# Performance work log

Hardware: AMD Instinct MI355X
Metric: run time of the kernel (lower is better)

## Reference

```python
import jax, jax.numpy as jnp
import numpy as np

B, T, DIM = 512, 243, 512
C = DIM // 2      # 256 channels per branch
CH = C // 2       # 128 hidden channels in ECL (cdiv=2)


def layer_norm(x, g, b, eps=1e-5):
    m = jnp.mean(x, axis=-1, keepdims=True)
    v = jnp.var(x, axis=-1, keepdims=True)
    return (x - m) * jax.lax.rsqrt(v + eps) * g + b


def gconv(x_btc, w):
    # grouped conv1d (groups=2), kernel 3, pad 1, no bias; x: [B,T,Cin], w: [Cout, Cin//2, 3]
    x = jnp.transpose(x_btc, (0, 2, 1))  # NCH
    y = jax.lax.conv_general_dilated(
        x, w, window_strides=(1,), padding=[(1, 1)],
        dimension_numbers=('NCH', 'OIH', 'NCH'), feature_group_count=2)
    return jnp.transpose(y, (0, 2, 1))


def setup_inputs() -> dict:
    key = jax.random.key(0)
    ks = jax.random.split(key, 4)
    F = (T + 1) // 2  # 122 == T//2+1 for odd T
    return {
        'x': jax.random.normal(ks[0], (B, T, DIM), dtype=jnp.float32),
        'lfilter': jax.random.normal(ks[1], (F, T // 2 + 1, 2), dtype=jnp.float32) * 0.02,
        'w1': jax.random.normal(ks[2], (CH, C // 2, 3), dtype=jnp.float32) * 0.05,
        'w2': jax.random.normal(ks[3], (C, CH // 2, 3), dtype=jnp.float32) * 0.05,
        'g1': jnp.ones((CH,), jnp.float32),
        'b1': jnp.zeros((CH,), jnp.float32),
        'g2': jnp.ones((C,), jnp.float32),
        'b2': jnp.zeros((C,), jnp.float32),
    }


def reference(x, lfilter, w1, w2, g1, b1, g2, b2):
    res, gate = jnp.split(x, 2, axis=-1)  # each [B, T, C]
    # GlobalFilter: rfft -> learned complex matmul over frequency axis -> irfft
    X = jnp.fft.rfft(res.astype(jnp.float32), n=T, axis=1, norm='ortho')  # [B, T//2+1, C] complex
    lf = lfilter[..., 0] + 1j * lfilter[..., 1]  # [(T+1)//2, T//2+1]
    X = jnp.einsum('fk,bkc->bfc', lf, X)
    res = jnp.fft.irfft(X, n=T, axis=1, norm='ortho')  # [B, T, C]
    # ECL gating branch
    h = gconv(gate, w1)                                  # [B, T, CH]
    h = jax.nn.gelu(layer_norm(h, g1, b1), approximate=False)
    h = gconv(h, w2)                                     # [B, T, C]
    h = jax.nn.sigmoid(layer_norm(h, g2, b2))
    gate = gate * h
    return jnp.concatenate([res, gate], axis=-1)
```

## Files before the change

### kernel.cpp

```cpp
#include <hip/hip_runtime.h>
#include <math.h>

typedef unsigned short ushort_t;
typedef unsigned int uint_t;
typedef __attribute__((ext_vector_type(8))) short short8v;
typedef __attribute__((ext_vector_type(4))) float f32x4;

#define BB   512
#define TT   243
#define DIMV 512
#define CC   256
#define CHH  128
#define FF   122
#define NKK  122

__device__ __forceinline__ float b2f(ushort_t u) {
  union { uint_t i; float f; } z; z.i = ((uint_t)u) << 16; return z.f;
}
__device__ __forceinline__ ushort_t f2b(float f) {
  union { float f; uint_t i; } z; z.f = f;
  uint_t r = (z.i + 0x7fffu + ((z.i >> 16) & 1u)) >> 16;
  return (ushort_t)r;
}
__device__ __forceinline__ uint_t pack2(float a, float b) {
  uint_t r;
  asm("v_cvt_pk_bf16_f32 %0, %1, %2" : "=v"(r) : "v"(a), "v"(b));
  return r;
}
__device__ __forceinline__ float gelu_f(float x) {
  float z = fabsf(x) * 0.70710678118654752f;
  float t = __builtin_amdgcn_rcpf(fmaf(0.3275911f, z, 1.0f));
  float p = fmaf(1.061405429f, t, -1.453152027f);
  p = fmaf(p, t, 1.421413741f);
  p = fmaf(p, t, -0.284496736f);
  p = fmaf(p, t, 0.254829592f);
  p = p * t;
  float e = __expf(-z * z);
  float erfa = 1.0f - p * e;
  float erfs = copysignf(erfa, x);
  return 0.5f * x * (1.0f + erfs);
}
__device__ __forceinline__ float sigmoid_f(float x) {
  return __builtin_amdgcn_rcpf(1.0f + __expf(-x));
}
union FragU { uint_t u[4]; short8v s; };


__global__ __launch_bounds__(256) void k_prep1(const float* __restrict__ lf, float* __restrict__ A,
    const float* __restrict__ w1, const float* __restrict__ w2,
    ushort_t* __restrict__ w1f, ushort_t* __restrict__ w2f) {
  __shared__ float2 tab[TT];
  int bid = blockIdx.x;
  if (bid < FF) {
    int f = bid;
    int tp = threadIdx.x;
    if (tp < TT) {
      float s, c;
      sincosf(6.28318530717958647692f * (float)tp / (float)TT, &s, &c);
      tab[tp] = make_float2(s, c);
    }
    __syncthreads();
    if (tp >= TT) return;
    float are = 0.f, aim = 0.f;
    int m = 0;
    const float* lrow = lf + (size_t)f * NKK * 2;
    for (int k = 0; k < NKK; ++k) {
      float2 sc = tab[m];
      float lr = lrow[2 * k], li = lrow[2 * k + 1];
      are = fmaf(lr, sc.y, fmaf(li, sc.x, are));
      aim = fmaf(li, sc.y, fmaf(-lr, sc.x, aim));
      m += tp; if (m >= TT) m -= TT;
    }
    A[(f * TT + tp) * 2 + 0] = are;
    A[(f * TT + tp) * 2 + 1] = aim;
  } else {
    int q = (bid - FF) * 256 + threadIdx.x;
    if (q < 49152) {
      int j = q & 7, l = (q >> 3) & 63, ot = (q >> 9) & 3, rest = q >> 11;
      int ks = rest % 12, g = rest / 12;
      int o = ot * 16 + (l & 15);
      int k = ks * 32 + 8 * (l >> 4) + j;
      int dk = k >> 7, i = k & 127;
      w1f[q] = f2b(w1[(g * 64 + o) * 384 + i * 3 + dk]);
    } else if (q < 98304) {
      int q2 = q - 49152;
      int j = q2 & 7, l = (q2 >> 3) & 63, ot = (q2 >> 9) & 7, rest = q2 >> 12;
      int ks = rest % 6, g = rest / 6;
      int o = ot * 16 + (l & 15);
      int k = ks * 32 + 8 * (l >> 4) + j;
      int dk = k >> 6, i = k & 63;
      w2f[q2] = f2b(w2[(g * 128 + o) * 192 + i * 3 + dk]);
    }
  }
}

__global__ void k_compute_M(const float* __restrict__ A, ushort_t* __restrict__ Ffrag) {
  __shared__ float2 tab[TT];
  int t = blockIdx.x;
  int tp = threadIdx.x;
  if (tp < TT) {
    float s, c;
    sincosf(6.28318530717958647692f * (float)tp / (float)TT, &s, &c);
    tab[tp] = make_float2(s, c);
  }
  __syncthreads();
  float val = 0.f;
  if (t < TT && tp < TT) {
    float acc = A[tp * 2 + 0];
    int m = t;
    for (int f = 1; f < FF; ++f) {
      float2 sc = tab[m];
      float ar = A[(f * TT + tp) * 2 + 0];
      float ai = A[(f * TT + tp) * 2 + 1];
      acc = fmaf(2.f * ar, sc.y, fmaf(-2.f * ai, sc.x, acc));
      m += t; if (m >= TT) m -= TT;
    }
    val = acc * (1.0f / (float)TT);
  }
  int kstep = tp >> 5, ko = tp & 31, p = ko >> 3, j = ko & 7;
  int mt = t >> 4, row = t & 15, lane = p * 16 + row;
  Ffrag[(((kstep * 16 + mt) * 64) + lane) * 8 + j] = f2b(val);
}


#define RST   129
#define BT    32
#define NTIL  8
#define XROWS 36
#define XSTD  130
#define HROWS 34
#define HSTD  66
#define GXS_OFF  0
#define GHS_OFF  4680
#define GRED_OFF 6924
#define SMEM_DW  8256

__device__ __forceinline__ void res_path(int rid, uint_t* smem,
    const float* __restrict__ x, const ushort_t* __restrict__ Ffrag, float* __restrict__ out) {
  uint_t* xs = smem;
  int b = rid >> 2, c0 = (rid & 3) * 64;
  int tid = threadIdx.x, l = tid & 63, w = tid >> 6;
  const float* xb = x + (size_t)b * TT * DIMV + c0;
  const short8v* Fp = (const short8v*)Ffrag;

  int cc = tid & 63, kp0 = tid >> 6;
#pragma unroll 8
  for (int it = 0; it < 32; ++it) {
    int kp = kp0 + 4 * it, tp = 2 * kp;
    float v0 = (tp < TT) ? xb[(size_t)tp * DIMV + cc] : 0.f;
    float v1 = (tp + 1 < TT) ? xb[(size_t)(tp + 1) * DIMV + cc] : 0.f;
    xs[cc * RST + kp] = pack2(v0, v1);
  }
  __syncthreads();

  f32x4 acc[4][4];
#pragma unroll
  for (int q = 0; q < 4; ++q)
#pragma unroll
    for (int m = 0; m < 4; ++m) acc[q][m] = (f32x4){0.f, 0.f, 0.f, 0.f};

#pragma unroll 2
  for (int ks = 0; ks < 8; ++ks) {
    FragU bfr[4];
#pragma unroll
    for (int q = 0; q < 4; ++q) bfr[q].s = Fp[(ks * 16 + 4 * w + q) * 64 + l];
#pragma unroll
    for (int m = 0; m < 4; ++m) {
      FragU af;
      const uint_t* pp = &xs[(16 * m + (l & 15)) * RST + ks * 16 + 4 * (l >> 4)];
      af.u[0] = pp[0]; af.u[1] = pp[1]; af.u[2] = pp[2]; af.u[3] = pp[3];
#pragma unroll
      for (int q = 0; q < 4; ++q)
        acc[q][m] = __builtin_amdgcn_mfma_f32_16x16x32_bf16(af.s, bfr[q].s, acc[q][m], 0, 0, 0);
    }
  }

  float* ob = out + (size_t)b * TT * DIMV + c0;
#pragma unroll
  for (int q = 0; q < 4; ++q) {
    int t = (4 * w + q) * 16 + (l & 15);
    if (t < TT) {
#pragma unroll
      for (int m = 0; m < 4; ++m)
        *(f32x4*)&ob[(size_t)t * DIMV + 16 * m + 4 * (l >> 4)] = acc[q][m];
    }
  }
}

__device__ __forceinline__ void gate_path(int gid, uint_t* smem,
    const float* __restrict__ x,
    const ushort_t* __restrict__ w1f, const float* __restrict__ g1, const float* __restrict__ b1,
    const ushort_t* __restrict__ w2f, const float* __restrict__ g2, const float* __restrict__ b2,
    float* __restrict__ out) {
  uint_t* xs = smem + GXS_OFF;
  uint_t* hs = smem + GHS_OFF;
  float* red1s = (float*)(smem + GRED_OFF);
  float* red1q = red1s + 192;
  float* red2s = red1q + 192;
  float* red2q = red2s + 128;
  int b = gid >> 3, t0 = (gid & 7) * BT;
  int tid = threadIdx.x, l = tid & 63, w = tid >> 6;
  int g = w >> 1, half = w & 1;

  const float* xb = x + (size_t)b * TT * DIMV + CC;
#pragma unroll 3
  for (int it = 0; it < 9; ++it) {
    int e = tid + it * 256;
    int r = e >> 6, cq = e & 63;
    int t = t0 - 2 + r;
    float4 v = make_float4(0.f, 0.f, 0.f, 0.f);
    if (t >= 0 && t < TT) v = *(const float4*)&xb[(size_t)t * DIMV + 4 * cq];
    *(uint2*)&xs[r * XSTD + 2 * cq] = make_uint2(pack2(v.x, v.y), pack2(v.z, v.w));
  }
  __syncthreads();

  const short8v* w1p = (const short8v*)w1f;
  int gdw = g * 64;
  f32x4 acc1[2][3];
#pragma unroll
  for (int a = 0; a < 2; ++a)
#pragma unroll
    for (int nt = 0; nt < 3; ++nt) acc1[a][nt] = (f32x4){0.f, 0.f, 0.f, 0.f};

#pragma unroll 2
  for (int ks = 0; ks < 12; ++ks) {
    short8v af[2];
#pragma unroll
    for (int a = 0; a < 2; ++a)
      af[a] = w1p[((g * 12 + ks) * 4 + half * 2 + a) * 64 + l];
    int dk = ks >> 2, i0dw = (ks & 3) * 16;
    FragU bf[3];
#pragma unroll
    for (int nt = 0; nt < 3; ++nt) {
      int row = (l & 15) + 16 * nt + dk;
      if (nt == 2) row = row > (XROWS - 1) ? (XROWS - 1) : row;
      const uint4* pp = (const uint4*)&xs[row * XSTD + gdw + i0dw + 4 * (l >> 4)];
      uint4 qv = *pp;
      bf[nt].u[0] = qv.x; bf[nt].u[1] = qv.y; bf[nt].u[2] = qv.z; bf[nt].u[3] = qv.w;
    }
#pragma unroll
    for (int a = 0; a < 2; ++a)
#pragma unroll
      for (int nt = 0; nt < 3; ++nt)
        acc1[a][nt] = __builtin_amdgcn_mfma_f32_16x16x32_bf16(af[a], bf[nt].s, acc1[a][nt], 0, 0, 0);
  }

#pragma unroll
  for (int nt = 0; nt < 3; ++nt) {
    float s = 0.f, s2 = 0.f;
#pragma unroll
    for (int a = 0; a < 2; ++a)
#pragma unroll
      for (int r = 0; r < 4; ++r) { float v = acc1[a][nt][r]; s += v; s2 += v * v; }
    s += __shfl_xor(s, 16); s += __shfl_xor(s, 32);
    s2 += __shfl_xor(s2, 16); s2 += __shfl_xor(s2, 32);
    if (l < 16) { red1s[w * 48 + l + 16 * nt] = s; red1q[w * 48 + l + 16 * nt] = s2; }
  }
  __syncthreads();

#pragma unroll
  for (int nt = 0; nt < 3; ++nt) {
    int c = (l & 15) + 16 * nt;
    if (c < HROWS) {
      int t_out = t0 - 1 + c;
      bool valid = (t_out >= 0 && t_out < TT);
      float S = red1s[0 * 48 + c] + red1s[1 * 48 + c] + red1s[2 * 48 + c] + red1s[3 * 48 + c];
      float S2 = red1q[0 * 48 + c] + red1q[1 * 48 + c] + red1q[2 * 48 + c] + red1q[3 * 48 + c];
      float mean = S * (1.f / 128.f);
      float var = S2 * (1.f / 128.f) - mean * mean;
      float rstd = rsqrtf(var + 1e-5f);
#pragma unroll
      for (int a = 0; a < 2; ++a) {
        int o0 = g * 64 + half * 32 + a * 16 + 4 * (l >> 4);
        float4 gg = *(const float4*)&g1[o0];
        float4 bb = *(const float4*)&b1[o0];
        float gv[4] = {gg.x, gg.y, gg.z, gg.w};
        float bv[4] = {bb.x, bb.y, bb.z, bb.w};
        float h4[4];
#pragma unroll
        for (int r = 0; r < 4; ++r) {
          float xn = (acc1[a][nt][r] - mean) * rstd * gv[r] + bv[r];
          h4[r] = valid ? gelu_f(xn) : 0.f;
        }
        *(uint2*)&hs[c * HSTD + (o0 >> 1)] =
            make_uint2(pack2(h4[0], h4[1]), pack2(h4[2], h4[3]));
      }
    }
  }
  __syncthreads();

  const short8v* w2p = (const short8v*)w2f;
  int gdw2 = g * 32;
  f32x4 acc2[4][2];
#pragma unroll
  for (int a = 0; a < 4; ++a)
#pragma unroll
    for (int nt = 0; nt < 2; ++nt) acc2[a][nt] = (f32x4){0.f, 0.f, 0.f, 0.f};

#pragma unroll 2
  for (int ks = 0; ks < 6; ++ks) {
    short8v af[4];
#pragma unroll
    for (int a = 0; a < 4; ++a)
      af[a] = w2p[((g * 6 + ks) * 8 + half * 4 + a) * 64 + l];
    int dk = ks >> 1, i0dw = (ks & 1) * 16;
    FragU bf[2];
#pragma unroll
    for (int nt = 0; nt < 2; ++nt) {
      int row = (l & 15) + 16 * nt + dk;
      const uint4* pp = (const uint4*)&hs[row * HSTD + gdw2 + i0dw + 4 * (l >> 4)];
      uint4 qv = *pp;
      bf[nt].u[0] = qv.x; bf[nt].u[1] = qv.y; bf[nt].u[2] = qv.z; bf[nt].u[3] = qv.w;
    }
#pragma unroll
    for (int a = 0; a < 4; ++a)
#pragma unroll
      for (int nt = 0; nt < 2; ++nt)
        acc2[a][nt] = __builtin_amdgcn_mfma_f32_16x16x32_bf16(af[a], bf[nt].s, acc2[a][nt], 0, 0, 0);
  }

#pragma unroll
  for (int nt = 0; nt < 2; ++nt) {
    float s = 0.f, s2 = 0.f;
#pragma unroll
    for (int a = 0; a < 4; ++a)
#pragma unroll
      for (int r = 0; r < 4; ++r) { float v = acc2[a][nt][r]; s += v; s2 += v * v; }
    s += __shfl_xor(s, 16); s += __shfl_xor(s, 32);
    s2 += __shfl_xor(s2, 16); s2 += __shfl_xor(s2, 32);
    if (l < 16) { red2s[w * 32 + l + 16 * nt] = s; red2q[w * 32 + l + 16 * nt] = s2; }
  }
  __syncthreads();

  float* ob = out + (size_t)b * TT * DIMV + CC;
#pragma unroll
  for (int nt = 0; nt < 2; ++nt) {
    int c = (l & 15) + 16 * nt;
    int t = t0 + c;
    if (t < TT) {
      float S = red2s[0 * 32 + c] + red2s[1 * 32 + c] + red2s[2 * 32 + c] + red2s[3 * 32 + c];
      float S2 = red2q[0 * 32 + c] + red2q[1 * 32 + c] + red2q[2 * 32 + c] + red2q[3 * 32 + c];
      float mean = S * (1.f / 256.f);
      float var = S2 * (1.f / 256.f) - mean * mean;
      float rstd = rsqrtf(var + 1e-5f);
      int xrow = c + 2;
#pragma unroll
      for (int a = 0; a < 4; ++a) {
        int o0 = g * 128 + (half * 4 + a) * 16 + 4 * (l >> 4);
        float4 gg = *(const float4*)&g2[o0];
        float4 bb = *(const float4*)&b2[o0];
        float gv[4] = {gg.x, gg.y, gg.z, gg.w};
        float bv[4] = {bb.x, bb.y, bb.z, bb.w};
        uint2 xv2 = *(const uint2*)&xs[xrow * XSTD + (o0 >> 1)];
        float xvv[4] = { b2f((ushort_t)(xv2.x & 0xffff)), b2f((ushort_t)(xv2.x >> 16)),
                         b2f((ushort_t)(xv2.y & 0xffff)), b2f((ushort_t)(xv2.y >> 16)) };
        f32x4 res;
#pragma unroll
        for (int r = 0; r < 4; ++r) {
          float xn = (acc2[a][nt][r] - mean) * rstd * gv[r] + bv[r];
          res[r] = xvv[r] * sigmoid_f(xn);
        }
        *(f32x4*)&ob[(size_t)t * DIMV + o0] = res;
      }
    }
  }
}

__global__ __launch_bounds__(256, 4) void k_main(const float* __restrict__ x,
    const ushort_t* __restrict__ Ffrag,
    const ushort_t* __restrict__ w1f, const float* __restrict__ g1, const float* __restrict__ b1,
    const ushort_t* __restrict__ w2f, const float* __restrict__ g2, const float* __restrict__ b2,
    float* __restrict__ out) {
  __shared__ uint_t smem[SMEM_DW];
  int bid = blockIdx.x;
  int k = bid / 3, r = bid - 3 * k;
  if (r == 0) {
    res_path(k, smem, x, Ffrag, out);
  } else {
    gate_path(2 * k + (r - 1), smem, x, w1f, g1, b1, w2f, g2, b2, out);
  }
}


extern "C" void kernel_launch(void* const* d_in, const int* in_sizes, int n_in,
                              void* d_out, int out_size, void* d_ws, size_t ws_size,
                              hipStream_t stream) {
  const float* x  = (const float*)d_in[0];
  const float* lf = (const float*)d_in[1];
  const float* w1 = (const float*)d_in[2];
  const float* w2 = (const float*)d_in[3];
  const float* g1 = (const float*)d_in[4];
  const float* b1 = (const float*)d_in[5];
  const float* g2 = (const float*)d_in[6];
  const float* b2 = (const float*)d_in[7];
  float* out = (float*)d_out;

  char* ws = (char*)d_ws;
  float*    A     = (float*)(ws);
  ushort_t* Ffrag = (ushort_t*)(ws + 262144);
  ushort_t* w1f   = (ushort_t*)(ws + 393216);
  ushort_t* w2f   = (ushort_t*)(ws + 491520);

  k_prep1<<<FF + 384, 256, 0, stream>>>(lf, A, w1, w2, w1f, w2f);
  k_compute_M<<<256, 256, 0, stream>>>(A, Ffrag);
  k_main<<<BB * 4 * 3, 256, 0, stream>>>(x, Ffrag, w1f, g1, b1, w2f, g2, b2, out);
}
```

Measured before the change: 241.4 us.

## Shrink shared memory and res tile to raise occupancy in fused kernel

The res path now handles 32 channels per block instead of 64, halving its accumulators and LDS tile, with the row stride reduced to 124. The gate path reuses one LDS region for the x and h tiles and rereads the gate input from global memory for the final multiply instead of keeping it in LDS. Together these cut shared memory from about 33KB to about 21KB, and launch bounds rise to 6 blocks per CU, with blocks interleaved 1:1 between res and gate. The trade-offs are one extra global read of the gate input per output, more blocks re-streaming the Ffrag matrix, and dropped unroll pragmas that may change instruction scheduling.

```diff
diff --git a/kernel.cpp b/kernel.cpp
--- a/kernel.cpp
+++ b/kernel.cpp
@@ -123,49 +123,48 @@
 }
 
 
-#define RST   129
+#define RST   124
 #define BT    32
-#define NTIL  8
 #define XROWS 36
 #define XSTD  130
 #define HROWS 34
 #define HSTD  66
-#define GXS_OFF  0
-#define GHS_OFF  4680
-#define GRED_OFF 6924
-#define SMEM_DW  8256
+#define GRED_OFF 4680
+#define SMEM_DW  5320
 
 __device__ __forceinline__ void res_path(int rid, uint_t* smem,
     const float* __restrict__ x, const ushort_t* __restrict__ Ffrag, float* __restrict__ out) {
   uint_t* xs = smem;
-  int b = rid >> 2, c0 = (rid & 3) * 64;
+  int b = rid >> 3, c0 = (rid & 7) * 32;
   int tid = threadIdx.x, l = tid & 63, w = tid >> 6;
   const float* xb = x + (size_t)b * TT * DIMV + c0;
   const short8v* Fp = (const short8v*)Ffrag;
 
-  int cc = tid & 63, kp0 = tid >> 6;
-#pragma unroll 8
-  for (int it = 0; it < 32; ++it) {
-    int kp = kp0 + 4 * it, tp = 2 * kp;
-    float v0 = (tp < TT) ? xb[(size_t)tp * DIMV + cc] : 0.f;
-    float v1 = (tp + 1 < TT) ? xb[(size_t)(tp + 1) * DIMV + cc] : 0.f;
-    xs[cc * RST + kp] = pack2(v0, v1);
-  }
-  __syncthreads();
-
-  f32x4 acc[4][4];
+  int cc = tid & 31, kq = tid >> 5;
+#pragma unroll
+  for (int it = 0; it < 16; ++it) {
+    int kp = kq + 8 * it;
+    if (kp < RST) {
+      int tp = 2 * kp;
+      float v0 = (tp < TT) ? xb[(size_t)tp * DIMV + cc] : 0.f;
+      float v1 = (tp + 1 < TT) ? xb[(size_t)(tp + 1) * DIMV + cc] : 0.f;
+      xs[cc * RST + kp] = pack2(v0, v1);
+    }
+  }
+  __syncthreads();
+
+  f32x4 acc[4][2];
 #pragma unroll
   for (int q = 0; q < 4; ++q)
 #pragma unroll
-    for (int m = 0; m < 4; ++m) acc[q][m] = (f32x4){0.f, 0.f, 0.f, 0.f};
-
-#pragma unroll 2
+    for (int m = 0; m < 2; ++m) acc[q][m] = (f32x4){0.f, 0.f, 0.f, 0.f};
+
   for (int ks = 0; ks < 8; ++ks) {
     FragU bfr[4];
 #pragma unroll
     for (int q = 0; q < 4; ++q) bfr[q].s = Fp[(ks * 16 + 4 * w + q) * 64 + l];
 #pragma unroll
-    for (int m = 0; m < 4; ++m) {
+    for (int m = 0; m < 2; ++m) {
       FragU af;
       const uint_t* pp = &xs[(16 * m + (l & 15)) * RST + ks * 16 + 4 * (l >> 4)];
       af.u[0] = pp[0]; af.u[1] = pp[1]; af.u[2] = pp[2]; af.u[3] = pp[3];
@@ -181,7 +180,7 @@
     int t = (4 * w + q) * 16 + (l & 15);
     if (t < TT) {
 #pragma unroll
-      for (int m = 0; m < 4; ++m)
+      for (int m = 0; m < 2; ++m)
         *(f32x4*)&ob[(size_t)t * DIMV + 16 * m + 4 * (l >> 4)] = acc[q][m];
     }
   }
@@ -192,8 +191,8 @@
     const ushort_t* __restrict__ w1f, const float* __restrict__ g1, const float* __restrict__ b1,
     const ushort_t* __restrict__ w2f, const float* __restrict__ g2, const float* __restrict__ b2,
     float* __restrict__ out) {
-  uint_t* xs = smem + GXS_OFF;
-  uint_t* hs = smem + GHS_OFF;
+  uint_t* xs = smem;
+  uint_t* hs = smem;
   float* red1s = (float*)(smem + GRED_OFF);
   float* red1q = red1s + 192;
   float* red2s = red1q + 192;
@@ -222,7 +221,6 @@
 #pragma unroll
     for (int nt = 0; nt < 3; ++nt) acc1[a][nt] = (f32x4){0.f, 0.f, 0.f, 0.f};
 
-#pragma unroll 2
   for (int ks = 0; ks < 12; ++ks) {
     short8v af[2];
 #pragma unroll
@@ -297,7 +295,6 @@
 #pragma unroll
     for (int nt = 0; nt < 2; ++nt) acc2[a][nt] = (f32x4){0.f, 0.f, 0.f, 0.f};
 
-#pragma unroll 2
   for (int ks = 0; ks < 6; ++ks) {
     short8v af[4];
 #pragma unroll
@@ -332,6 +329,7 @@
   }
   __syncthreads();
 
+  const float* xg = x + (size_t)b * TT * DIMV + CC;
   float* ob = out + (size_t)b * TT * DIMV + CC;
 #pragma unroll
   for (int nt = 0; nt < 2; ++nt) {
@@ -343,7 +341,6 @@
       float mean = S * (1.f / 256.f);
       float var = S2 * (1.f / 256.f) - mean * mean;
       float rstd = rsqrtf(var + 1e-5f);
-      int xrow = c + 2;
 #pragma unroll
       for (int a = 0; a < 4; ++a) {
         int o0 = g * 128 + (half * 4 + a) * 16 + 4 * (l >> 4);
@@ -351,9 +348,8 @@
         float4 bb = *(const float4*)&b2[o0];
         float gv[4] = {gg.x, gg.y, gg.z, gg.w};
         float bv[4] = {bb.x, bb.y, bb.z, bb.w};
-        uint2 xv2 = *(const uint2*)&xs[xrow * XSTD + (o0 >> 1)];
-        float xvv[4] = { b2f((ushort_t)(xv2.x & 0xffff)), b2f((ushort_t)(xv2.x >> 16)),
-                         b2f((ushort_t)(xv2.y & 0xffff)), b2f((ushort_t)(xv2.y >> 16)) };
+        float4 xv = *(const float4*)&xg[(size_t)t * DIMV + o0];
+        float xvv[4] = {xv.x, xv.y, xv.z, xv.w};
         f32x4 res;
 #pragma unroll
         for (int r = 0; r < 4; ++r) {
@@ -366,18 +362,17 @@
   }
 }
 
-__global__ __launch_bounds__(256, 4) void k_main(const float* __restrict__ x,
+__global__ __launch_bounds__(256, 6) void k_main(const float* __restrict__ x,
     const ushort_t* __restrict__ Ffrag,
     const ushort_t* __restrict__ w1f, const float* __restrict__ g1, const float* __restrict__ b1,
     const ushort_t* __restrict__ w2f, const float* __restrict__ g2, const float* __restrict__ b2,
     float* __restrict__ out) {
   __shared__ uint_t smem[SMEM_DW];
   int bid = blockIdx.x;
-  int k = bid / 3, r = bid - 3 * k;
-  if (r == 0) {
-    res_path(k, smem, x, Ffrag, out);
+  if (bid & 1) {
+    gate_path(bid >> 1, smem, x, w1f, g1, b1, w2f, g2, b2, out);
   } else {
-    gate_path(2 * k + (r - 1), smem, x, w1f, g1, b1, w2f, g2, b2, out);
+    res_path(bid >> 1, smem, x, Ffrag, out);
   }
 }
 
@@ -403,5 +398,5 @@
 
   k_prep1<<<FF + 384, 256, 0, stream>>>(lf, A, w1, w2, w1f, w2f);
   k_compute_M<<<256, 256, 0, stream>>>(A, Ffrag);
-  k_main<<<BB * 4 * 3, 256, 0, stream>>>(x, Ffrag, w1f, g1, b1, w2f, g2, b2, out);
-}
+  k_main<<<BB * 8 * 2, 256, 0, stream>>>(x, Ffrag, w1f, g1, b1, w2f, g2, b2, out);
+}
```

Result: slower. 290.2 us (+20.2%).
